# Kernel optimization log

Measured on AMD Instinct MI355X. Metric: run time of the kernel, lower is better.

## Reference

```python
import jax, jax.numpy as jnp
import numpy as np

LOG2PI = float(np.log(2.0 * np.pi))
MIN_DURATION = 1
NUM_STATES = 512
OBS_DIM = 128
B, T, K = 64, 2000, 400


def setup_inputs() -> dict:
    key = jax.random.key(0)
    ks = jax.random.split(key, 10)
    observations = jax.random.normal(ks[0], (B, T, OBS_DIM), dtype=jnp.float32)
    state_sequence = jax.random.randint(ks[1], (B, K), 0, NUM_STATES, dtype=jnp.int32)
    # durations >= min_duration so gamma log-prob stays finite
    duration_sequence = jax.random.randint(ks[2], (B, K), 1, 51, dtype=jnp.int32)
    # learned parameters, initialized as in the torch module
    alpha_params = jnp.ones((NUM_STATES,), jnp.float32)
    beta_params = jnp.ones((NUM_STATES,), jnp.float32)
    transition_logits = jax.random.normal(ks[3], (NUM_STATES, NUM_STATES), dtype=jnp.float32)
    initial_logits = jnp.zeros((NUM_STATES,), jnp.float32)
    observation_means = jax.random.normal(ks[4], (NUM_STATES, OBS_DIM), dtype=jnp.float32)
    observation_logvars = jnp.zeros((NUM_STATES, OBS_DIM), jnp.float32)
    return {
        "observations": observations,
        "alpha_params": alpha_params,
        "beta_params": beta_params,
        "transition_logits": transition_logits,
        "initial_logits": initial_logits,
        "observation_means": observation_means,
        "observation_logvars": observation_logvars,
        "state_sequence": state_sequence,
        "duration_sequence": duration_sequence,
    }


def _gamma_duration_logprob(alpha_params, beta_params, state_sequence, duration_sequence):
    # fully vectorized version of the per-sample Python loop in DurationModel
    d = duration_sequence.astype(jnp.float32)                      # [B, K]
    alpha = jax.nn.softplus(alpha_params)[state_sequence] + 1e-6   # [B, K]
    beta = jax.nn.softplus(beta_params)[state_sequence] + 1e-6
    lp = (alpha - 1.0) * jnp.log(d + 1e-8) - beta * d
    lp = lp - (jax.lax.lgamma(alpha) - alpha * jnp.log(beta))
    return jnp.where(d >= MIN_DURATION, lp, -jnp.inf)


def reference(observations, alpha_params, beta_params, transition_logits,
              initial_logits, observation_means, observation_logvars,
              state_sequence, duration_sequence):
    # --- duration log-probs per segment: [B, K]
    log_dur = _gamma_duration_logprob(alpha_params, beta_params,
                                      state_sequence, duration_sequence)

    # --- expand segments to frames: frame t belongs to segment with cum[idx-1] <= t < cum[idx]
    cum = jnp.cumsum(duration_sequence, axis=1)                    # [B, K]
    t = jnp.arange(observations.shape[1])                          # [T]
    seg_idx = jax.vmap(lambda c: jnp.searchsorted(c, t, side='right'))(cum)
    seg_idx = jnp.clip(seg_idx, 0, state_sequence.shape[1] - 1)    # [B, T]
    frame_states = jnp.take_along_axis(state_sequence, seg_idx, axis=1)  # [B, T]

    # --- diagonal-gaussian observation log-probs per frame: [B, T]
    mu = observation_means[frame_states]                           # [B, T, D]
    lv = observation_logvars[frame_states]                         # [B, T, D]
    resid2 = (observations - mu) ** 2 * jnp.exp(-lv)
    log_obs = -0.5 * jnp.sum(lv + resid2 + LOG2PI, axis=-1)        # [B, T]

    # --- initial + transition log-probs over the segment-level state chain
    log_trans = jax.nn.log_softmax(transition_logits, axis=-1)     # [S, S]
    log_init = jax.nn.log_softmax(initial_logits)                  # [S]
    trans_lp = log_trans[state_sequence[:, :-1], state_sequence[:, 1:]].sum(axis=1)  # [B]
    init_lp = log_init[state_sequence[:, 0]]                       # [B]

    # --- per-sequence supervised log-likelihood: [B]
    log_likelihood = log_obs.sum(axis=1) + log_dur.sum(axis=1) + trans_lp + init_lp
    return log_likelihood
```

## Files before the change

### kernel.cpp

```cpp
#include <hip/hip_runtime.h>
#include <hip/hip_bf16.h>
#include <math.h>

#define NS 512
#define OD 128
#define BB 64
#define TT 2000
#define KK 400
#define CHUNK 128
#define NCH 16
#define LOG2PI_F 1.8378770664093453f
#define PART_OFF 4096
#define SEQ_OFF  5632


__device__ __forceinline__ float softplusf(float x) {
    return (x > 20.f) ? x : log1pf(expf(x));
}

__global__ __launch_bounds__(256) void big_kernel(
    const float* __restrict__ obs, const float* __restrict__ mu,
    const float* __restrict__ lvar, const float* __restrict__ trans,
    const float* __restrict__ init_logits,
    const float* __restrict__ alpha_p, const float* __restrict__ beta_p,
    const int* __restrict__ states, const int* __restrict__ durs,
    float* __restrict__ ws)
{
    const int tid = threadIdx.x;
    const int bid = blockIdx.x;
    __shared__ float red[4];

    if (bid < BB * NCH) {
        const int b = bid >> 4;
        const int t0 = (bid & 15) * CHUNK;

        __shared__ int st[KK];
        __shared__ int cum[512];
        __shared__ int csum[8];
        __shared__ int fsl[CHUNK];

        const int lane = tid & 63, w = tid >> 6;
        int v0 = 0, v1 = 0;
        if (tid < KK) { st[tid] = states[b * KK + tid]; v0 = durs[b * KK + tid]; }
        if (tid + 256 < KK) { st[tid + 256] = states[b * KK + tid + 256];
                              v1 = durs[b * KK + tid + 256]; }
        #pragma unroll
        for (int off = 1; off < 64; off <<= 1) {
            int u0 = __shfl_up(v0, off, 64);
            int u1 = __shfl_up(v1, off, 64);
            if (lane >= off) { v0 += u0; v1 += u1; }
        }
        if (lane == 63) { csum[w] = v0; csum[4 + w] = v1; }
        __syncthreads();
        int off0 = 0, off1 = 0;
        #pragma unroll
        for (int c = 0; c < 8; ++c) {
            int cs = csum[c];
            off0 += (c < w) ? cs : 0;
            off1 += (c < 4 + w) ? cs : 0;
        }
        cum[tid] = v0 + off0;
        cum[tid + 256] = v1 + off1;
        __syncthreads();

        if (tid < CHUNK) {
            const int t = t0 + tid;
            int lo = 0, hi = KK;
            while (lo < hi) {
                int mid = (lo + hi) >> 1;
                if (cum[mid] <= t) lo = mid + 1; else hi = mid;
            }
            fsl[tid] = st[(lo > KK - 1) ? (KK - 1) : lo];
        }
        __syncthreads();

        const int row = tid >> 5;
        const int d = (tid & 31) * 4;
        float acc = 0.f;
        #pragma unroll
        for (int i = 0; i < CHUNK / 8; ++i) {
            const int t = t0 + i * 8 + row;
            if (t < TT) {
                const int s = fsl[i * 8 + row];
                const float4 o  = *(const float4*)(obs + ((size_t)(b * TT + t)) * OD + d);
                const float4 m  = *(const float4*)(mu  + (size_t)s * OD + d);
                const float4 lv = *(const float4*)(lvar + (size_t)s * OD + d);
                const float dx = o.x - m.x, dy = o.y - m.y, dz = o.z - m.z, dw = o.w - m.w;
                acc += lv.x + lv.y + lv.z + lv.w + 4.f * LOG2PI_F
                     + dx * dx * __expf(-lv.x) + dy * dy * __expf(-lv.y)
                     + dz * dz * __expf(-lv.z) + dw * dw * __expf(-lv.w);
            }
        }
        for (int off = 32; off; off >>= 1) acc += __shfl_down(acc, off, 64);
        if ((tid & 63) == 0) red[tid >> 6] = acc;
        __syncthreads();
        if (tid == 0)
            ws[PART_OFF + bid] = red[0] + red[1] + red[2] + red[3];
    } else if (bid < BB * NCH + NS + 1) {
        const int r = bid - BB * NCH;
        const float* src = (r < NS) ? (trans + (size_t)r * NS) : init_logits;
        float x0 = src[tid];
        float x1 = src[tid + 256];
        float m = fmaxf(x0, x1);
        for (int off = 32; off; off >>= 1) m = fmaxf(m, __shfl_down(m, off, 64));
        if ((tid & 63) == 0) red[tid >> 6] = m;
        __syncthreads();
        m = fmaxf(fmaxf(red[0], red[1]), fmaxf(red[2], red[3]));
        __syncthreads();
        float e = __expf(x0 - m) + __expf(x1 - m);
        for (int off = 32; off; off >>= 1) e += __shfl_down(e, off, 64);
        if ((tid & 63) == 0) red[tid >> 6] = e;
        __syncthreads();
        if (tid == 0)
            ws[(r < NS) ? r : 512] = m + __logf(red[0] + red[1] + red[2] + red[3]);
    } else {
        const int b = bid - (BB * NCH + NS + 1);
        float lp = 0.f;
        for (int k = tid; k < KK; k += 256) {
            const int s = states[b * KK + k];
            const float dv = (float)durs[b * KK + k];
            const float a  = softplusf(alpha_p[s]) + 1e-6f;
            const float bt = softplusf(beta_p[s]) + 1e-6f;
            float v = (a - 1.f) * __logf(dv + 1e-8f) - bt * dv
                    + a * __logf(bt) - lgammaf(a);
            lp += (dv >= 1.f) ? v : -INFINITY;
            if (k < KK - 1)
                lp += trans[(size_t)s * NS + states[b * KK + k + 1]];
        }
        for (int off = 32; off; off >>= 1) lp += __shfl_down(lp, off, 64);
        if ((tid & 63) == 0) red[tid >> 6] = lp;
        __syncthreads();
        if (tid == 0)
            ws[SEQ_OFF + b] = red[0] + red[1] + red[2] + red[3];
    }
}

__global__ __launch_bounds__(256) void fin_kernel(
    const float* __restrict__ init_logits, const int* __restrict__ states,
    const float* __restrict__ ws, float* __restrict__ out)
{
    const int b = blockIdx.x;
    const int tid = threadIdx.x;
    __shared__ float red[4];

    float lp = 0.f;
    if (tid < NCH)        lp = -0.5f * ws[PART_OFF + b * NCH + tid];
    else if (tid == NCH)  lp = ws[SEQ_OFF + b];
    for (int k = tid; k < KK - 1; k += 256)
        lp -= ws[states[b * KK + k]];
    for (int off = 32; off; off >>= 1) lp += __shfl_down(lp, off, 64);
    if ((tid & 63) == 0) red[tid >> 6] = lp;
    __syncthreads();
    if (tid == 0)
        out[b] = red[0] + red[1] + red[2] + red[3]
               + init_logits[states[b * KK]] - ws[512];
}

extern "C" void kernel_launch(void* const* d_in, const int* in_sizes, int n_in,
                              void* d_out, int out_size, void* d_ws, size_t ws_size,
                              hipStream_t stream) {
    const float* observations = (const float*)d_in[0];
    const float* alpha_p      = (const float*)d_in[1];
    const float* beta_p       = (const float*)d_in[2];
    const float* trans        = (const float*)d_in[3];
    const float* init_logits  = (const float*)d_in[4];
    const float* obs_means    = (const float*)d_in[5];
    const float* obs_logvars  = (const float*)d_in[6];
    const int*   state_seq    = (const int*)d_in[7];
    const int*   dur_seq      = (const int*)d_in[8];

    float* ws = (float*)d_ws;
    float* out = (float*)d_out;

    big_kernel<<<BB * NCH + NS + 1 + BB, 256, 0, stream>>>(
        observations, obs_means, obs_logvars, trans, init_logits,
        alpha_p, beta_p, state_seq, dur_seq, ws);
    fin_kernel<<<BB, 256, 0, stream>>>(init_logits, state_seq, ws, out);
}
```

Before: 22.21 us.

## Split small reductions into first kernel and fuse final reduce via last-block atomic

Moves the transition/initial log-softmax and the per-sequence duration/transition work into a small first kernel. The heavy observation kernel then runs second and uses a per-sequence atomic counter so the last chunk block does the final reduction, which removes the separate finalize kernel. It also adds a fast path with no bounds check for full chunks. The trade-off is that the two kernels now run in sequence, so the small kernel's latency lands on the critical path instead of overlapping with the big one. Correctness relies on the counters being zeroed by the first kernel each call.

```diff
diff --git a/kernel.cpp b/kernel.cpp
--- a/kernel.cpp
+++ b/kernel.cpp
@@ -10,18 +10,17 @@
 #define CHUNK 128
 #define NCH 16
 #define LOG2PI_F 1.8378770664093453f
-#define PART_OFF 4096
-#define SEQ_OFF  5632
+#define SEQ_OFF  576
+#define CNT_OFF  640
+#define PART_OFF 1024
 
 
 __device__ __forceinline__ float softplusf(float x) {
     return (x > 20.f) ? x : log1pf(expf(x));
 }
 
-__global__ __launch_bounds__(256) void big_kernel(
-    const float* __restrict__ obs, const float* __restrict__ mu,
-    const float* __restrict__ lvar, const float* __restrict__ trans,
-    const float* __restrict__ init_logits,
+__global__ __launch_bounds__(256) void k1_kernel(
+    const float* __restrict__ trans, const float* __restrict__ init_logits,
     const float* __restrict__ alpha_p, const float* __restrict__ beta_p,
     const int* __restrict__ states, const int* __restrict__ durs,
     float* __restrict__ ws)
@@ -30,53 +29,116 @@
     const int bid = blockIdx.x;
     __shared__ float red[4];
 
-    if (bid < BB * NCH) {
-        const int b = bid >> 4;
-        const int t0 = (bid & 15) * CHUNK;
-
-        __shared__ int st[KK];
-        __shared__ int cum[512];
-        __shared__ int csum[8];
-        __shared__ int fsl[CHUNK];
-
-        const int lane = tid & 63, w = tid >> 6;
-        int v0 = 0, v1 = 0;
-        if (tid < KK) { st[tid] = states[b * KK + tid]; v0 = durs[b * KK + tid]; }
-        if (tid + 256 < KK) { st[tid + 256] = states[b * KK + tid + 256];
-                              v1 = durs[b * KK + tid + 256]; }
+    if (bid <= NS) {
+        const float* src = (bid < NS) ? (trans + (size_t)bid * NS) : init_logits;
+        float x0 = src[tid];
+        float x1 = src[tid + 256];
+        float m = fmaxf(x0, x1);
+        for (int off = 32; off; off >>= 1) m = fmaxf(m, __shfl_down(m, off, 64));
+        if ((tid & 63) == 0) red[tid >> 6] = m;
+        __syncthreads();
+        m = fmaxf(fmaxf(red[0], red[1]), fmaxf(red[2], red[3]));
+        __syncthreads();
+        float e = __expf(x0 - m) + __expf(x1 - m);
+        for (int off = 32; off; off >>= 1) e += __shfl_down(e, off, 64);
+        if ((tid & 63) == 0) red[tid >> 6] = e;
+        __syncthreads();
+        if (tid == 0)
+            ws[(bid < NS) ? bid : 512] = m + __logf(red[0] + red[1] + red[2] + red[3]);
+    } else {
+        const int b = bid - (NS + 1);
+        if (tid == 0) ((int*)ws)[CNT_OFF + b] = 0;
+        float lp = 0.f;
+        for (int k = tid; k < KK; k += 256) {
+            const int s = states[b * KK + k];
+            const float dv = (float)durs[b * KK + k];
+            const float a  = softplusf(alpha_p[s]) + 1e-6f;
+            const float bt = softplusf(beta_p[s]) + 1e-6f;
+            float v = (a - 1.f) * __logf(dv + 1e-8f) - bt * dv
+                    + a * __logf(bt) - lgammaf(a);
+            lp += (dv >= 1.f) ? v : -INFINITY;
+            if (k < KK - 1)
+                lp += trans[(size_t)s * NS + states[b * KK + k + 1]];
+        }
+        for (int off = 32; off; off >>= 1) lp += __shfl_down(lp, off, 64);
+        if ((tid & 63) == 0) red[tid >> 6] = lp;
+        __syncthreads();
+        if (tid == 0)
+            ws[SEQ_OFF + b] = red[0] + red[1] + red[2] + red[3]
+                            + init_logits[states[b * KK]];
+    }
+}
+
+__global__ __launch_bounds__(256) void k2_kernel(
+    const float* __restrict__ obs, const float* __restrict__ mu,
+    const float* __restrict__ lvar,
+    const int* __restrict__ states, const int* __restrict__ durs,
+    float* __restrict__ ws, float* __restrict__ out)
+{
+    const int tid = threadIdx.x;
+    const int bid = blockIdx.x;
+    const int b = bid >> 4;
+    const int t0 = (bid & 15) * CHUNK;
+
+    __shared__ float red[4];
+    __shared__ int st[KK];
+    __shared__ int cum[512];
+    __shared__ int csum[8];
+    __shared__ int fsl[CHUNK];
+    __shared__ int sh_last;
+
+    const int lane = tid & 63, w = tid >> 6;
+    int v0 = 0, v1 = 0;
+    if (tid < KK) { st[tid] = states[b * KK + tid]; v0 = durs[b * KK + tid]; }
+    if (tid + 256 < KK) { st[tid + 256] = states[b * KK + tid + 256];
+                          v1 = durs[b * KK + tid + 256]; }
+    #pragma unroll
+    for (int off = 1; off < 64; off <<= 1) {
+        int u0 = __shfl_up(v0, off, 64);
+        int u1 = __shfl_up(v1, off, 64);
+        if (lane >= off) { v0 += u0; v1 += u1; }
+    }
+    if (lane == 63) { csum[w] = v0; csum[4 + w] = v1; }
+    __syncthreads();
+    int off0 = 0, off1 = 0;
+    #pragma unroll
+    for (int c = 0; c < 8; ++c) {
+        int cs = csum[c];
+        off0 += (c < w) ? cs : 0;
+        off1 += (c < 4 + w) ? cs : 0;
+    }
+    cum[tid] = v0 + off0;
+    cum[tid + 256] = v1 + off1;
+    __syncthreads();
+
+    if (tid < CHUNK) {
+        const int t = t0 + tid;
+        int lo = 0, hi = KK;
+        while (lo < hi) {
+            int mid = (lo + hi) >> 1;
+            if (cum[mid] <= t) lo = mid + 1; else hi = mid;
+        }
+        fsl[tid] = st[(lo > KK - 1) ? (KK - 1) : lo];
+    }
+    __syncthreads();
+
+    const int row = tid >> 5;
+    const int d = (tid & 31) * 4;
+    float acc = 0.f;
+    if (t0 + CHUNK <= TT) {
         #pragma unroll
-        for (int off = 1; off < 64; off <<= 1) {
-            int u0 = __shfl_up(v0, off, 64);
-            int u1 = __shfl_up(v1, off, 64);
-            if (lane >= off) { v0 += u0; v1 += u1; }
-        }
-        if (lane == 63) { csum[w] = v0; csum[4 + w] = v1; }
-        __syncthreads();
-        int off0 = 0, off1 = 0;
-        #pragma unroll
-        for (int c = 0; c < 8; ++c) {
-            int cs = csum[c];
-            off0 += (c < w) ? cs : 0;
-            off1 += (c < 4 + w) ? cs : 0;
-        }
-        cum[tid] = v0 + off0;
-        cum[tid + 256] = v1 + off1;
-        __syncthreads();
-
-        if (tid < CHUNK) {
-            const int t = t0 + tid;
-            int lo = 0, hi = KK;
-            while (lo < hi) {
-                int mid = (lo + hi) >> 1;
-                if (cum[mid] <= t) lo = mid + 1; else hi = mid;
-            }
-            fsl[tid] = st[(lo > KK - 1) ? (KK - 1) : lo];
-        }
-        __syncthreads();
-
-        const int row = tid >> 5;
-        const int d = (tid & 31) * 4;
-        float acc = 0.f;
+        for (int i = 0; i < CHUNK / 8; ++i) {
+            const int t = t0 + i * 8 + row;
+            const int s = fsl[i * 8 + row];
+            const float4 o  = *(const float4*)(obs + ((size_t)(b * TT + t)) * OD + d);
+            const float4 m  = *(const float4*)(mu  + (size_t)s * OD + d);
+            const float4 lv = *(const float4*)(lvar + (size_t)s * OD + d);
+            const float dx = o.x - m.x, dy = o.y - m.y, dz = o.z - m.z, dw = o.w - m.w;
+            acc += lv.x + lv.y + lv.z + lv.w + 4.f * LOG2PI_F
+                 + dx * dx * __expf(-lv.x) + dy * dy * __expf(-lv.y)
+                 + dz * dz * __expf(-lv.z) + dw * dw * __expf(-lv.w);
+        }
+    } else {
         #pragma unroll
         for (int i = 0; i < CHUNK / 8; ++i) {
             const int t = t0 + i * 8 + row;
@@ -91,69 +153,31 @@
                      + dz * dz * __expf(-lv.z) + dw * dw * __expf(-lv.w);
             }
         }
-        for (int off = 32; off; off >>= 1) acc += __shfl_down(acc, off, 64);
-        if ((tid & 63) == 0) red[tid >> 6] = acc;
-        __syncthreads();
-        if (tid == 0)
-            ws[PART_OFF + bid] = red[0] + red[1] + red[2] + red[3];
-    } else if (bid < BB * NCH + NS + 1) {
-        const int r = bid - BB * NCH;
-        const float* src = (r < NS) ? (trans + (size_t)r * NS) : init_logits;
-        float x0 = src[tid];
-        float x1 = src[tid + 256];
-        float m = fmaxf(x0, x1);
-        for (int off = 32; off; off >>= 1) m = fmaxf(m, __shfl_down(m, off, 64));
-        if ((tid & 63) == 0) red[tid >> 6] = m;
-        __syncthreads();
-        m = fmaxf(fmaxf(red[0], red[1]), fmaxf(red[2], red[3]));
-        __syncthreads();
-        float e = __expf(x0 - m) + __expf(x1 - m);
-        for (int off = 32; off; off >>= 1) e += __shfl_down(e, off, 64);
-        if ((tid & 63) == 0) red[tid >> 6] = e;
-        __syncthreads();
-        if (tid == 0)
-            ws[(r < NS) ? r : 512] = m + __logf(red[0] + red[1] + red[2] + red[3]);
-    } else {
-        const int b = bid - (BB * NCH + NS + 1);
+    }
+    for (int off = 32; off; off >>= 1) acc += __shfl_down(acc, off, 64);
+    if ((tid & 63) == 0) red[tid >> 6] = acc;
+    __syncthreads();
+    if (tid == 0) {
+        ws[PART_OFF + bid] = -0.5f * (red[0] + red[1] + red[2] + red[3]);
+        __threadfence();
+        int old = atomicAdd(&((int*)ws)[CNT_OFF + b], 1);
+        sh_last = (old == NCH - 1);
+    }
+    __syncthreads();
+
+    if (sh_last) {
+        __threadfence();
         float lp = 0.f;
-        for (int k = tid; k < KK; k += 256) {
-            const int s = states[b * KK + k];
-            const float dv = (float)durs[b * KK + k];
-            const float a  = softplusf(alpha_p[s]) + 1e-6f;
-            const float bt = softplusf(beta_p[s]) + 1e-6f;
-            float v = (a - 1.f) * __logf(dv + 1e-8f) - bt * dv
-                    + a * __logf(bt) - lgammaf(a);
-            lp += (dv >= 1.f) ? v : -INFINITY;
-            if (k < KK - 1)
-                lp += trans[(size_t)s * NS + states[b * KK + k + 1]];
-        }
+        if (tid < NCH)       lp = ws[PART_OFF + b * NCH + tid];
+        else if (tid == NCH) lp = ws[SEQ_OFF + b] - ws[512];
+        for (int k = tid; k < KK - 1; k += 256)
+            lp -= ws[st[k]];
         for (int off = 32; off; off >>= 1) lp += __shfl_down(lp, off, 64);
         if ((tid & 63) == 0) red[tid >> 6] = lp;
         __syncthreads();
         if (tid == 0)
-            ws[SEQ_OFF + b] = red[0] + red[1] + red[2] + red[3];
-    }
-}
-
-__global__ __launch_bounds__(256) void fin_kernel(
-    const float* __restrict__ init_logits, const int* __restrict__ states,
-    const float* __restrict__ ws, float* __restrict__ out)
-{
-    const int b = blockIdx.x;
-    const int tid = threadIdx.x;
-    __shared__ float red[4];
-
-    float lp = 0.f;
-    if (tid < NCH)        lp = -0.5f * ws[PART_OFF + b * NCH + tid];
-    else if (tid == NCH)  lp = ws[SEQ_OFF + b];
-    for (int k = tid; k < KK - 1; k += 256)
-        lp -= ws[states[b * KK + k]];
-    for (int off = 32; off; off >>= 1) lp += __shfl_down(lp, off, 64);
-    if ((tid & 63) == 0) red[tid >> 6] = lp;
-    __syncthreads();
-    if (tid == 0)
-        out[b] = red[0] + red[1] + red[2] + red[3]
-               + init_logits[states[b * KK]] - ws[512];
+            out[b] = red[0] + red[1] + red[2] + red[3];
+    }
 }
 
 extern "C" void kernel_launch(void* const* d_in, const int* in_sizes, int n_in,
@@ -172,8 +196,8 @@
     float* ws = (float*)d_ws;
     float* out = (float*)d_out;
 
-    big_kernel<<<BB * NCH + NS + 1 + BB, 256, 0, stream>>>(
-        observations, obs_means, obs_logvars, trans, init_logits,
-        alpha_p, beta_p, state_seq, dur_seq, ws);
-    fin_kernel<<<BB, 256, 0, stream>>>(init_logits, state_seq, ws, out);
-}
+    k1_kernel<<<NS + 1 + BB, 256, 0, stream>>>(
+        trans, init_logits, alpha_p, beta_p, state_seq, dur_seq, ws);
+    k2_kernel<<<BB * NCH, 256, 0, stream>>>(
+        observations, obs_means, obs_logvars, state_seq, dur_seq, ws, out);
+}
```

Result: slower. 74.48 us (+235.3%).
